# Kernel optimization log

Hardware: AMD Instinct MI355X
Metric: run time of the kernel (lower is better)

Reference implementation:

```python
import jax, jax.numpy as jnp
import numpy as np

T, B, I, H, P = 256, 128, 1024, 1024, 512  # seq, batch, input, hidden, proj


def setup_inputs() -> dict:
    key = jax.random.key(0)
    ks = jax.random.split(key, 6)
    s = 1.0 / np.sqrt(H)  # torch LSTM init bound: uniform(-1/sqrt(H), 1/sqrt(H))
    x = jax.random.normal(ks[0], (T, B, I), dtype=jnp.float32)
    h = jax.random.normal(ks[1], (1, B, P), dtype=jnp.float32) * 0.1
    c = jax.random.normal(ks[2], (1, B, H), dtype=jnp.float32) * 0.1
    W_ih = jax.random.uniform(ks[3], (4 * H, I), minval=-s, maxval=s, dtype=jnp.float32)
    W_hh = jax.random.uniform(ks[4], (4 * H, P), minval=-s, maxval=s, dtype=jnp.float32)
    W_hr = jax.random.uniform(ks[5], (P, H), minval=-s, maxval=s, dtype=jnp.float32)
    return {"x": x, "h": h, "c": c, "W_ih": W_ih, "W_hh": W_hh, "W_hr": W_hr}


def _lstm_proj(x, h0, c0, W_ih, W_hh, W_hr):
    # Precompute input contribution to gates for all timesteps: [T,B,4H]
    xg = jnp.einsum('tbi,gi->tbg', x, W_ih)

    def step(carry, xg_t):
        h_t, c_t = carry  # h_t:[B,P], c_t:[B,H]
        gates = xg_t + h_t @ W_hh.T  # [B,4H]
        i, f, g, o = jnp.split(gates, 4, axis=-1)  # torch gate order: i,f,g,o
        i = jax.nn.sigmoid(i)
        f = jax.nn.sigmoid(f)
        g = jnp.tanh(g)
        o = jax.nn.sigmoid(o)
        c_new = f * c_t + i * g
        h_full = o * jnp.tanh(c_new)        # [B,H]
        h_new = h_full @ W_hr.T             # projection -> [B,P]
        return (h_new, c_new), h_new

    (hT, cT), ys = jax.lax.scan(step, (h0[0], c0[0]), xg)
    return ys, hT[None, :, :], cT[None, :, :]


def reference(x, h, c, W_ih, W_hh, W_hr):
    return _lstm_proj(x, h, c, W_ih, W_hh, W_hr)
```

## Files before the change

kernel.cpp:

```cpp
#include <hip/hip_runtime.h>
#include <hip/hip_bf16.h>

#define TS 256
#define BB 128
#define II 1024
#define HH 1024
#define PP 512
#define GG 4096
#define NWG 256
#define WPG 64
#define BT 32
#define HCW 16
#define BSTRIDE 1032
#define RSTRIDE 20
#define SMEM_BYTES (64 * BSTRIDE * 2 + 2 * 64 * RSTRIDE * 4)

typedef __attribute__((ext_vector_type(8))) short bf16x8;
typedef __attribute__((ext_vector_type(4))) float f32x4;

__device__ __forceinline__ short f2bs(float f) {
    __hip_bfloat16 h = __float2bfloat16(f);
    return __builtin_bit_cast(short, h);
}
__device__ __forceinline__ float bs2f(short s) {
    return __bfloat162float(__builtin_bit_cast(__hip_bfloat16, s));
}

__device__ __forceinline__ bf16x8 ld8(const __hip_bfloat16* p) {
    return *(const bf16x8*)p;
}
__device__ __forceinline__ bf16x8 ld8(const float* p) {
    f32x4 lo = *(const f32x4*)p;
    f32x4 hi = *(const f32x4*)(p + 4);
    bf16x8 r;
#pragma unroll
    for (int i = 0; i < 4; ++i) { r[i] = f2bs(lo[i]); r[4 + i] = f2bs(hi[i]); }
    return r;
}

__device__ __forceinline__ void stv(float* p, long i, float v) { p[i] = v; }
__device__ __forceinline__ void stv(__hip_bfloat16* p, long i, float v) { p[i] = __float2bfloat16(v); }

__device__ __forceinline__ void st_bf16_wt(__hip_bfloat16* p, float v) {
    int si = (int)f2bs(v);
    asm volatile("global_store_short %0, %1, off sc1" :: "v"(p), "v"(si));
}
__device__ __forceinline__ f32x4 ld16_mall(const void* p) {
    f32x4 r;
    asm volatile("global_load_dwordx4 %0, %1, off sc1" : "=&v"(r) : "v"(p));
    return r;
}
__device__ __forceinline__ void vm_drain() {
    asm volatile("s_waitcnt vmcnt(0)" ::: "memory");
}

template <typename AT, typename BT_, typename CT>
__global__ __launch_bounds__(256) void mfma_gemm_bt(const AT* __restrict__ A,
                                                    const BT_* __restrict__ B,
                                                    CT* __restrict__ C,
                                                    int M, int N, int K) {
    __shared__ __align__(16) short As[128][40];
    __shared__ __align__(16) short Bsh[128][40];
    const int tid = threadIdx.x;
    const long bm = (long)blockIdx.y * 128;
    const long bn = (long)blockIdx.x * 128;
    const int lane = tid & 63, wv = tid >> 6;
    const int l15 = lane & 15, quad = lane >> 4;
    const int wm = (wv >> 1) * 64, wn = (wv & 1) * 64;
    f32x4 acc[4][4] = {};
    for (int k0 = 0; k0 < K; k0 += 32) {
#pragma unroll
        for (int i = 0; i < 2; ++i) {
            int ch = tid + 256 * i;
            int row = ch >> 2, koff = (ch & 3) * 8;
            *(bf16x8*)&As[row][koff] = ld8(&A[(bm + row) * (long)K + k0 + koff]);
            *(bf16x8*)&Bsh[row][koff] = ld8(&B[(bn + row) * (long)K + k0 + koff]);
        }
        __syncthreads();
        bf16x8 af[4], bfv[4];
#pragma unroll
        for (int t = 0; t < 4; ++t) {
            af[t] = *(const bf16x8*)&As[wm + t * 16 + l15][quad * 8];
            bfv[t] = *(const bf16x8*)&Bsh[wn + t * 16 + l15][quad * 8];
        }
#pragma unroll
        for (int mt = 0; mt < 4; ++mt)
#pragma unroll
            for (int nt = 0; nt < 4; ++nt)
                acc[mt][nt] = __builtin_amdgcn_mfma_f32_16x16x32_bf16(af[mt], bfv[nt], acc[mt][nt], 0, 0, 0);
        __syncthreads();
    }
#pragma unroll
    for (int mt = 0; mt < 4; ++mt)
#pragma unroll
        for (int nt = 0; nt < 4; ++nt)
#pragma unroll
            for (int r = 0; r < 4; ++r) {
                long row = bm + wm + mt * 16 + quad * 4 + r;
                long col = bn + wn + nt * 16 + l15;
                stv(C, row * N + col, acc[mt][nt][r]);
            }
}

template <int K>
__device__ __forceinline__ void rec_mm(const __hip_bfloat16* __restrict__ Abase,
                                       const short* __restrict__ Bs, f32x4* acc,
                                       int l15, int quad, int mt, int kh) {
    constexpr int KH = K / 2;
    constexpr int NI = KH / 32;
    const __hip_bfloat16* ap = Abase + (long)(mt * 16 + l15) * K + kh * KH + quad * 8;
    const short* bp0 = Bs + l15 * BSTRIDE + kh * KH + quad * 8;
    f32x4 avr[NI];
#pragma unroll
    for (int i = 0; i < NI; ++i) avr[i] = ld16_mall(ap + i * 32);
    asm volatile("s_waitcnt vmcnt(0)" ::: "memory");
    __builtin_amdgcn_sched_barrier(0);
#pragma unroll
    for (int i = 0; i < NI; ++i) {
        bf16x8 av = __builtin_bit_cast(bf16x8, avr[i]);
        const short* bp = bp0 + i * 32;
        acc[0] = __builtin_amdgcn_mfma_f32_16x16x32_bf16(av, *(const bf16x8*)(bp), acc[0], 0, 0, 0);
        acc[1] = __builtin_amdgcn_mfma_f32_16x16x32_bf16(av, *(const bf16x8*)(bp + 16 * BSTRIDE), acc[1], 0, 0, 0);
        acc[2] = __builtin_amdgcn_mfma_f32_16x16x32_bf16(av, *(const bf16x8*)(bp + 32 * BSTRIDE), acc[2], 0, 0, 0);
        acc[3] = __builtin_amdgcn_mfma_f32_16x16x32_bf16(av, *(const bf16x8*)(bp + 48 * BSTRIDE), acc[3], 0, 0, 0);
    }
}

__global__ __launch_bounds__(256) void lstm_rec_k(
    const __hip_bfloat16* __restrict__ h0b,
    const float* __restrict__ c0,
    const float* __restrict__ Whh,
    const __hip_bfloat16* __restrict__ Wcomb,
    const __hip_bfloat16* __restrict__ xg,
    __hip_bfloat16* __restrict__ hfull,
    float* __restrict__ cT,
    unsigned* __restrict__ flags) {
    extern __shared__ char smem[];
    short* Bs = (short*)smem;
    float* red = (float*)(smem + 64 * BSTRIDE * 2);

    const int tid = threadIdx.x;
    const int wg = blockIdx.x;
    const int grp = wg >> 6;
    const int jj = wg & 63;
    const int hc0 = jj * HCW;
    const int bt = grp * BT;
    const int lane = tid & 63, wv = tid >> 6;
    const int l15 = lane & 15, quad = lane >> 4;
    const int mt = wv & 1, kh = wv >> 1;
    unsigned* gflag = flags + grp * (2 * WPG);
    const int brow = bt + mt * 16 + quad * 4;

    for (int ch = tid; ch < 64 * 64; ch += 256) {
        int row = ch >> 6, koff = (ch & 63) * 8;
        long wr = (long)(row >> 4) * HH + hc0 + (row & 15);
        *(bf16x8*)&Bs[row * BSTRIDE + koff] = ld8(&Whh[wr * PP + koff]);
    }

    float creg[4];
    if (kh == 0) {
#pragma unroll
        for (int r = 0; r < 4; ++r) creg[r] = c0[(long)(brow + r) * HH + hc0 + l15];
    }

    short xr[16];
    auto ldxg = [&](int t) {
        if (kh == 0) {
            const __hip_bfloat16* xgt = xg + (long)t * BB * GG;
#pragma unroll
            for (int g = 0; g < 4; ++g)
#pragma unroll
                for (int r = 0; r < 4; ++r)
                    xr[g * 4 + r] = *(const short*)(xgt + (long)(brow + r) * GG + g * HH + hc0 + l15);
        }
    };

    auto wave_wait = [&](int want) {
        const unsigned* fp = gflag + mt * WPG + kh * 32;
        for (;;) {
            unsigned v = __hip_atomic_load(&fp[lane & 31], __ATOMIC_RELAXED,
                                           __HIP_MEMORY_SCOPE_AGENT);
            if (__all((int)(v >= (unsigned)want))) break;
            __builtin_amdgcn_s_sleep(1);
        }
    };

    auto finish = [&](f32x4* acc, int t, bool flag) {
        if (kh == 1) {
            float* rp = red + (mt * 64 + lane) * RSTRIDE;
#pragma unroll
            for (int g = 0; g < 4; ++g) *(f32x4*)(rp + g * 4) = acc[g];
        }
        __syncthreads();
        if (kh == 0) {
            const float* rp = red + (mt * 64 + lane) * RSTRIDE;
#pragma unroll
            for (int g = 0; g < 4; ++g) acc[g] += *(const f32x4*)(rp + g * 4);
            __hip_bfloat16* hp = hfull + (long)t * BB * HH;
#pragma unroll
            for (int r = 0; r < 4; ++r) {
                float gi = acc[0][r] + bs2f(xr[r]);
                float gf = acc[1][r] + bs2f(xr[4 + r]);
                float gg = acc[2][r] + bs2f(xr[8 + r]);
                float go = acc[3][r] + bs2f(xr[12 + r]);
                float i_ = 1.f / (1.f + expf(-gi));
                float f_ = 1.f / (1.f + expf(-gf));
                float g_ = tanhf(gg);
                float o_ = 1.f / (1.f + expf(-go));
                float c = f_ * creg[r] + i_ * g_;
                creg[r] = c;
                st_bf16_wt(hp + (long)(brow + r) * HH + hc0 + l15, o_ * tanhf(c));
            }
            vm_drain();
            if (flag && lane == 0) {
                __hip_atomic_store(&gflag[mt * WPG + jj], (unsigned)(t + 1),
                                   __ATOMIC_RELAXED, __HIP_MEMORY_SCOPE_AGENT);
            }
        }
    };

    ldxg(0);
    __syncthreads();
    {
        f32x4 acc[4] = {};
        rec_mm<PP>(h0b + (long)bt * PP, Bs, acc, l15, quad, mt, kh);
        finish(acc, 0, true);
    }
    for (int ch = tid; ch < 64 * 128; ch += 256) {
        int row = ch >> 7, koff = (ch & 127) * 8;
        long wr = (long)(row >> 4) * HH + hc0 + (row & 15);
        *(bf16x8*)&Bs[row * BSTRIDE + koff] = *(const bf16x8*)&Wcomb[wr * HH + koff];
    }
    __syncthreads();

    for (int t = 1; t < TS; ++t) {
        ldxg(t);
        wave_wait(t);
        f32x4 acc[4] = {};
        rec_mm<HH>(hfull + ((long)(t - 1) * BB + bt) * HH, Bs, acc, l15, quad, mt, kh);
        finish(acc, t, t < TS - 1);
    }

    if (kh == 0) {
#pragma unroll
        for (int r = 0; r < 4; ++r) cT[(long)(brow + r) * HH + hc0 + l15] = creg[r];
    }
}

__global__ __launch_bounds__(256) void prep_k(const float* __restrict__ h0,
                                              __hip_bfloat16* __restrict__ h0b,
                                              const float* __restrict__ Whr,
                                              float* __restrict__ WhrT,
                                              unsigned* __restrict__ flags) {
    int i = blockIdx.x * 256 + threadIdx.x;
    if (i < 2 * NWG) flags[i] = 0u;
    if (i < BB * PP) h0b[i] = __float2bfloat16(h0[i]);
    if (i < PP * HH) {
        int h = i / PP, p = i % PP;
        WhrT[i] = Whr[(long)p * HH + h];
    }
}

__global__ __launch_bounds__(256) void tail_k(const float* __restrict__ ys_last,
                                              float* __restrict__ hT) {
    int i = blockIdx.x * 256 + threadIdx.x;
    hT[i] = ys_last[i];
}

extern "C" void kernel_launch(void* const* d_in, const int* in_sizes, int n_in,
                              void* d_out, int out_size, void* d_ws, size_t ws_size,
                              hipStream_t stream) {
    const float* x   = (const float*)d_in[0];
    const float* h0  = (const float*)d_in[1];
    const float* c0  = (const float*)d_in[2];
    const float* Wih = (const float*)d_in[3];
    const float* Whh = (const float*)d_in[4];
    const float* Whr = (const float*)d_in[5];

    float* out = (float*)d_out;
    float* ys = out;
    float* hT = out + (long)TS * BB * PP;
    float* cT = hT + (long)BB * PP;

    char* ws = (char*)d_ws;
    size_t off = 0;
    __hip_bfloat16* xg = (__hip_bfloat16*)(ws + off);    off += (size_t)TS * BB * GG * 2;
    __hip_bfloat16* hfull = (__hip_bfloat16*)(ws + off); off += (size_t)TS * BB * HH * 2;
    __hip_bfloat16* Wcomb = (__hip_bfloat16*)(ws + off); off += (size_t)GG * HH * 2;
    float* WhrT = (float*)(ws + off);                    off += (size_t)HH * PP * 4;
    __hip_bfloat16* h0b = (__hip_bfloat16*)(ws + off);   off += (size_t)BB * PP * 2;
    unsigned* flags = (unsigned*)(ws + off);             off += 4096;

    static int smem_inited = 0;
    if (!smem_inited) {
        (void)hipFuncSetAttribute(reinterpret_cast<const void*>(lstm_rec_k),
                                  hipFuncAttributeMaxDynamicSharedMemorySize, SMEM_BYTES);
        smem_inited = 1;
    }

    dim3 blk(256);

    prep_k<<<dim3((PP * HH) / 256), blk, 0, stream>>>(h0, h0b, Whr, WhrT, flags);

    mfma_gemm_bt<float, float, __hip_bfloat16>
        <<<dim3(GG / 128, (TS * BB) / 128), blk, 0, stream>>>(x, Wih, xg, TS * BB, GG, II);

    mfma_gemm_bt<float, float, __hip_bfloat16>
        <<<dim3(HH / 128, GG / 128), blk, 0, stream>>>(Whh, WhrT, Wcomb, GG, HH, PP);

    {
        const __hip_bfloat16* a0 = h0b;
        const float* a1 = c0;
        const float* a2 = Whh;
        const __hip_bfloat16* a3 = Wcomb;
        const __hip_bfloat16* a4 = xg;
        __hip_bfloat16* a5 = hfull;
        float* a6 = cT;
        unsigned* a7 = flags;
        void* args[] = {(void*)&a0, (void*)&a1, (void*)&a2, (void*)&a3,
                        (void*)&a4, (void*)&a5, (void*)&a6, (void*)&a7};
        (void)hipLaunchCooperativeKernel(reinterpret_cast<void*>(lstm_rec_k),
                                         dim3(NWG), blk, args, SMEM_BYTES, stream);
    }

    mfma_gemm_bt<__hip_bfloat16, float, float>
        <<<dim3(PP / 128, (TS * BB) / 128), blk, 0, stream>>>(hfull, Whr, ys, TS * BB, PP, HH);

    tail_k<<<dim3((BB * PP) / 256), blk, 0, stream>>>(ys + (long)(TS - 1) * BB * PP, hT);
}
```

Before: 2.813 ms.

## Halve recurrent workgroups and drop split-K reduction with per-wave full-K rows

The persistent recurrent kernel now runs 128 workgroups in two batch groups of 64 rows instead of 256 workgroups in four groups. Each wave owns 16 batch rows and the full K dimension, so the LDS split-K reduction and the per-step __syncthreads go away, and each wave waits only on its own flags. Cache-policy bits on the h stores and loads also change from sc1 to sc0 sc1. The trade-off is twice the MFMA and load work per wave and half as many CUs in use, in exchange for less synchronisation on the serial critical path.

```diff
diff --git a/kernel.cpp b/kernel.cpp
--- a/kernel.cpp
+++ b/kernel.cpp
@@ -7,13 +7,14 @@
 #define HH 1024
 #define PP 512
 #define GG 4096
-#define NWG 256
+#define NWG 128
+#define NGRP 2
 #define WPG 64
-#define BT 32
+#define BT 64
 #define HCW 16
 #define BSTRIDE 1032
-#define RSTRIDE 20
-#define SMEM_BYTES (64 * BSTRIDE * 2 + 2 * 64 * RSTRIDE * 4)
+#define NFLAGS (NGRP * 4 * WPG)
+#define SMEM_BYTES (64 * BSTRIDE * 2)
 
 typedef __attribute__((ext_vector_type(8))) short bf16x8;
 typedef __attribute__((ext_vector_type(4))) float f32x4;
@@ -43,11 +44,11 @@
 
 __device__ __forceinline__ void st_bf16_wt(__hip_bfloat16* p, float v) {
     int si = (int)f2bs(v);
-    asm volatile("global_store_short %0, %1, off sc1" :: "v"(p), "v"(si));
+    asm volatile("global_store_short %0, %1, off sc0 sc1" :: "v"(p), "v"(si));
 }
 __device__ __forceinline__ f32x4 ld16_mall(const void* p) {
     f32x4 r;
-    asm volatile("global_load_dwordx4 %0, %1, off sc1" : "=&v"(r) : "v"(p));
+    asm volatile("global_load_dwordx4 %0, %1, off sc0 sc1" : "=&v"(r) : "v"(p));
     return r;
 }
 __device__ __forceinline__ void vm_drain() {
@@ -102,28 +103,11 @@
             }
 }
 
-template <int K>
-__device__ __forceinline__ void rec_mm(const __hip_bfloat16* __restrict__ Abase,
-                                       const short* __restrict__ Bs, f32x4* acc,
-                                       int l15, int quad, int mt, int kh) {
-    constexpr int KH = K / 2;
-    constexpr int NI = KH / 32;
-    const __hip_bfloat16* ap = Abase + (long)(mt * 16 + l15) * K + kh * KH + quad * 8;
-    const short* bp0 = Bs + l15 * BSTRIDE + kh * KH + quad * 8;
-    f32x4 avr[NI];
-#pragma unroll
-    for (int i = 0; i < NI; ++i) avr[i] = ld16_mall(ap + i * 32);
-    asm volatile("s_waitcnt vmcnt(0)" ::: "memory");
-    __builtin_amdgcn_sched_barrier(0);
-#pragma unroll
-    for (int i = 0; i < NI; ++i) {
-        bf16x8 av = __builtin_bit_cast(bf16x8, avr[i]);
-        const short* bp = bp0 + i * 32;
-        acc[0] = __builtin_amdgcn_mfma_f32_16x16x32_bf16(av, *(const bf16x8*)(bp), acc[0], 0, 0, 0);
-        acc[1] = __builtin_amdgcn_mfma_f32_16x16x32_bf16(av, *(const bf16x8*)(bp + 16 * BSTRIDE), acc[1], 0, 0, 0);
-        acc[2] = __builtin_amdgcn_mfma_f32_16x16x32_bf16(av, *(const bf16x8*)(bp + 32 * BSTRIDE), acc[2], 0, 0, 0);
-        acc[3] = __builtin_amdgcn_mfma_f32_16x16x32_bf16(av, *(const bf16x8*)(bp + 48 * BSTRIDE), acc[3], 0, 0, 0);
-    }
+__device__ __forceinline__ void mfma4(bf16x8 av, const short* bp, f32x4* acc) {
+    acc[0] = __builtin_amdgcn_mfma_f32_16x16x32_bf16(av, *(const bf16x8*)(bp), acc[0], 0, 0, 0);
+    acc[1] = __builtin_amdgcn_mfma_f32_16x16x32_bf16(av, *(const bf16x8*)(bp + 16 * BSTRIDE), acc[1], 0, 0, 0);
+    acc[2] = __builtin_amdgcn_mfma_f32_16x16x32_bf16(av, *(const bf16x8*)(bp + 32 * BSTRIDE), acc[2], 0, 0, 0);
+    acc[3] = __builtin_amdgcn_mfma_f32_16x16x32_bf16(av, *(const bf16x8*)(bp + 48 * BSTRIDE), acc[3], 0, 0, 0);
 }
 
 __global__ __launch_bounds__(256) void lstm_rec_k(
@@ -137,7 +121,6 @@
     unsigned* __restrict__ flags) {
     extern __shared__ char smem[];
     short* Bs = (short*)smem;
-    float* red = (float*)(smem + 64 * BSTRIDE * 2);
 
     const int tid = threadIdx.x;
     const int wg = blockIdx.x;
@@ -147,9 +130,10 @@
     const int bt = grp * BT;
     const int lane = tid & 63, wv = tid >> 6;
     const int l15 = lane & 15, quad = lane >> 4;
-    const int mt = wv & 1, kh = wv >> 1;
-    unsigned* gflag = flags + grp * (2 * WPG);
-    const int brow = bt + mt * 16 + quad * 4;
+    unsigned* fbase = flags + grp * (4 * WPG) + wv * WPG;
+    const int brow = bt + wv * 16 + quad * 4;
+    const int arow = bt + wv * 16 + l15;
+    const short* bp0 = Bs + l15 * BSTRIDE + quad * 8;
 
     for (int ch = tid; ch < 64 * 64; ch += 256) {
         int row = ch >> 6, koff = (ch & 63) * 8;
@@ -158,27 +142,22 @@
     }
 
     float creg[4];
-    if (kh == 0) {
-#pragma unroll
-        for (int r = 0; r < 4; ++r) creg[r] = c0[(long)(brow + r) * HH + hc0 + l15];
-    }
+#pragma unroll
+    for (int r = 0; r < 4; ++r) creg[r] = c0[(long)(brow + r) * HH + hc0 + l15];
 
     short xr[16];
     auto ldxg = [&](int t) {
-        if (kh == 0) {
-            const __hip_bfloat16* xgt = xg + (long)t * BB * GG;
-#pragma unroll
-            for (int g = 0; g < 4; ++g)
-#pragma unroll
-                for (int r = 0; r < 4; ++r)
-                    xr[g * 4 + r] = *(const short*)(xgt + (long)(brow + r) * GG + g * HH + hc0 + l15);
-        }
+        const __hip_bfloat16* xgt = xg + (long)t * BB * GG;
+#pragma unroll
+        for (int g = 0; g < 4; ++g)
+#pragma unroll
+            for (int r = 0; r < 4; ++r)
+                xr[g * 4 + r] = *(const short*)(xgt + (long)(brow + r) * GG + g * HH + hc0 + l15);
     };
 
     auto wave_wait = [&](int want) {
-        const unsigned* fp = gflag + mt * WPG + kh * 32;
         for (;;) {
-            unsigned v = __hip_atomic_load(&fp[lane & 31], __ATOMIC_RELAXED,
+            unsigned v = __hip_atomic_load(&fbase[lane], __ATOMIC_RELAXED,
                                            __HIP_MEMORY_SCOPE_AGENT);
             if (__all((int)(v >= (unsigned)want))) break;
             __builtin_amdgcn_s_sleep(1);
@@ -186,46 +165,48 @@
     };
 
     auto finish = [&](f32x4* acc, int t, bool flag) {
-        if (kh == 1) {
-            float* rp = red + (mt * 64 + lane) * RSTRIDE;
-#pragma unroll
-            for (int g = 0; g < 4; ++g) *(f32x4*)(rp + g * 4) = acc[g];
-        }
-        __syncthreads();
-        if (kh == 0) {
-            const float* rp = red + (mt * 64 + lane) * RSTRIDE;
-#pragma unroll
-            for (int g = 0; g < 4; ++g) acc[g] += *(const f32x4*)(rp + g * 4);
-            __hip_bfloat16* hp = hfull + (long)t * BB * HH;
-#pragma unroll
-            for (int r = 0; r < 4; ++r) {
-                float gi = acc[0][r] + bs2f(xr[r]);
-                float gf = acc[1][r] + bs2f(xr[4 + r]);
-                float gg = acc[2][r] + bs2f(xr[8 + r]);
-                float go = acc[3][r] + bs2f(xr[12 + r]);
-                float i_ = 1.f / (1.f + expf(-gi));
-                float f_ = 1.f / (1.f + expf(-gf));
-                float g_ = tanhf(gg);
-                float o_ = 1.f / (1.f + expf(-go));
-                float c = f_ * creg[r] + i_ * g_;
-                creg[r] = c;
-                st_bf16_wt(hp + (long)(brow + r) * HH + hc0 + l15, o_ * tanhf(c));
-            }
-            vm_drain();
-            if (flag && lane == 0) {
-                __hip_atomic_store(&gflag[mt * WPG + jj], (unsigned)(t + 1),
-                                   __ATOMIC_RELAXED, __HIP_MEMORY_SCOPE_AGENT);
-            }
-        }
+        __hip_bfloat16* hp = hfull + (long)t * BB * HH + (long)brow * HH + hc0 + l15;
+#pragma unroll
+        for (int r = 0; r < 4; ++r) {
+            float gi = acc[0][r] + bs2f(xr[r]);
+            float gf = acc[1][r] + bs2f(xr[4 + r]);
+            float gg = acc[2][r] + bs2f(xr[8 + r]);
+            float go = acc[3][r] + bs2f(xr[12 + r]);
+            float i_ = 1.f / (1.f + expf(-gi));
+            float f_ = 1.f / (1.f + expf(-gf));
+            float g_ = tanhf(gg);
+            float o_ = 1.f / (1.f + expf(-go));
+            float c = f_ * creg[r] + i_ * g_;
+            creg[r] = c;
+            st_bf16_wt(hp + (long)r * HH, o_ * tanhf(c));
+        }
+        vm_drain();
+        if (flag && lane == 0) {
+            __hip_atomic_store(&fbase[jj], (unsigned)(t + 1),
+                               __ATOMIC_RELAXED, __HIP_MEMORY_SCOPE_AGENT);
+        }
+    };
+
+    auto a_phase = [&](const __hip_bfloat16* ap, int c0_, f32x4* acc) {
+        f32x4 avr[16];
+#pragma unroll
+        for (int i = 0; i < 16; ++i) avr[i] = ld16_mall(ap + (c0_ + i) * 32);
+        asm volatile("s_waitcnt vmcnt(0)" ::: "memory");
+        __builtin_amdgcn_sched_barrier(0);
+#pragma unroll
+        for (int i = 0; i < 16; ++i)
+            mfma4(__builtin_bit_cast(bf16x8, avr[i]), bp0 + (c0_ + i) * 32, acc);
+        __builtin_amdgcn_sched_barrier(0);
     };
 
     ldxg(0);
     __syncthreads();
     {
         f32x4 acc[4] = {};
-        rec_mm<PP>(h0b + (long)bt * PP, Bs, acc, l15, quad, mt, kh);
+        a_phase(h0b + (long)arow * PP + quad * 8, 0, acc);
         finish(acc, 0, true);
     }
+    __syncthreads();
     for (int ch = tid; ch < 64 * 128; ch += 256) {
         int row = ch >> 7, koff = (ch & 127) * 8;
         long wr = (long)(row >> 4) * HH + hc0 + (row & 15);
@@ -236,15 +217,15 @@
     for (int t = 1; t < TS; ++t) {
         ldxg(t);
         wave_wait(t);
+        const __hip_bfloat16* ap = hfull + ((long)(t - 1) * BB + arow) * HH + quad * 8;
         f32x4 acc[4] = {};
-        rec_mm<HH>(hfull + ((long)(t - 1) * BB + bt) * HH, Bs, acc, l15, quad, mt, kh);
+        a_phase(ap, 0, acc);
+        a_phase(ap, 16, acc);
         finish(acc, t, t < TS - 1);
     }
 
-    if (kh == 0) {
-#pragma unroll
-        for (int r = 0; r < 4; ++r) cT[(long)(brow + r) * HH + hc0 + l15] = creg[r];
-    }
+#pragma unroll
+    for (int r = 0; r < 4; ++r) cT[(long)(brow + r) * HH + hc0 + l15] = creg[r];
 }
 
 __global__ __launch_bounds__(256) void prep_k(const float* __restrict__ h0,
@@ -253,7 +234,7 @@
                                               float* __restrict__ WhrT,
                                               unsigned* __restrict__ flags) {
     int i = blockIdx.x * 256 + threadIdx.x;
-    if (i < 2 * NWG) flags[i] = 0u;
+    if (i < NFLAGS) flags[i] = 0u;
     if (i < BB * PP) h0b[i] = __float2bfloat16(h0[i]);
     if (i < PP * HH) {
         int h = i / PP, p = i % PP;
```

New measurement: 3.421 ms. 21.6% more time.

## Remap recurrent workgroups across XCDs, pad h buffer, and use coherent loads

Applied to the files above, without the earlier changes.

Workgroup IDs are remapped so that each batch group's workgroups are interleaved across the chip's dies (bid&7 picks the group). The per-timestep hidden-state buffer is padded with an extra stride so consecutive timesteps do not alias. The cache-policy bits on the cross-workgroup h stores and loads are changed: stores now use sc0 sc1 and loads become plain global loads, with an acquire fence added at kernel start. The GEMM takes an explicit A tile stride so it can read the padded layout. It also adds some dead creg code. This risks coherence problems because the plain loads may hit stale L2 lines across dies.

```diff
diff --git a/kernel.cpp b/kernel.cpp
--- a/kernel.cpp
+++ b/kernel.cpp
@@ -8,11 +8,14 @@
 #define PP 512
 #define GG 4096
 #define NWG 256
+#define NGRP 4
 #define WPG 64
 #define BT 32
 #define HCW 16
 #define BSTRIDE 1032
 #define RSTRIDE 20
+#define HSTRIDE (BB * HH + 1024)
+#define NFLAGS (NGRP * 2 * WPG)
 #define SMEM_BYTES (64 * BSTRIDE * 2 + 2 * 64 * RSTRIDE * 4)
 
 typedef __attribute__((ext_vector_type(8))) short bf16x8;
@@ -43,11 +46,11 @@
 
 __device__ __forceinline__ void st_bf16_wt(__hip_bfloat16* p, float v) {
     int si = (int)f2bs(v);
-    asm volatile("global_store_short %0, %1, off sc1" :: "v"(p), "v"(si));
-}
-__device__ __forceinline__ f32x4 ld16_mall(const void* p) {
+    asm volatile("global_store_short %0, %1, off sc0 sc1" :: "v"(p), "v"(si));
+}
+__device__ __forceinline__ f32x4 ld16c(const void* p) {
     f32x4 r;
-    asm volatile("global_load_dwordx4 %0, %1, off sc1" : "=&v"(r) : "v"(p));
+    asm volatile("global_load_dwordx4 %0, %1, off" : "=&v"(r) : "v"(p));
     return r;
 }
 __device__ __forceinline__ void vm_drain() {
@@ -58,10 +61,12 @@
 __global__ __launch_bounds__(256) void mfma_gemm_bt(const AT* __restrict__ A,
                                                     const BT_* __restrict__ B,
                                                     CT* __restrict__ C,
-                                                    int M, int N, int K) {
+                                                    int M, int N, int K,
+                                                    long AtileStride) {
     __shared__ __align__(16) short As[128][40];
     __shared__ __align__(16) short Bsh[128][40];
     const int tid = threadIdx.x;
+    const long abase = (long)blockIdx.y * AtileStride;
     const long bm = (long)blockIdx.y * 128;
     const long bn = (long)blockIdx.x * 128;
     const int lane = tid & 63, wv = tid >> 6;
@@ -73,7 +78,7 @@
         for (int i = 0; i < 2; ++i) {
             int ch = tid + 256 * i;
             int row = ch >> 2, koff = (ch & 3) * 8;
-            *(bf16x8*)&As[row][koff] = ld8(&A[(bm + row) * (long)K + k0 + koff]);
+            *(bf16x8*)&As[row][koff] = ld8(&A[abase + row * (long)K + k0 + koff]);
             *(bf16x8*)&Bsh[row][koff] = ld8(&B[(bn + row) * (long)K + k0 + koff]);
         }
         __syncthreads();
@@ -112,7 +117,7 @@
     const short* bp0 = Bs + l15 * BSTRIDE + kh * KH + quad * 8;
     f32x4 avr[NI];
 #pragma unroll
-    for (int i = 0; i < NI; ++i) avr[i] = ld16_mall(ap + i * 32);
+    for (int i = 0; i < NI; ++i) avr[i] = ld16c(ap + i * 32);
     asm volatile("s_waitcnt vmcnt(0)" ::: "memory");
     __builtin_amdgcn_sched_barrier(0);
 #pragma unroll
@@ -139,10 +144,13 @@
     short* Bs = (short*)smem;
     float* red = (float*)(smem + 64 * BSTRIDE * 2);
 
+    __builtin_amdgcn_fence(__ATOMIC_ACQUIRE, "agent");
+
     const int tid = threadIdx.x;
-    const int wg = blockIdx.x;
-    const int grp = wg >> 6;
-    const int jj = wg & 63;
+    const int bid = blockIdx.x;
+    const int x8 = bid & 7;
+    const int grp = x8 >> 1;
+    const int jj = ((bid >> 3) << 1) | (x8 & 1);
     const int hc0 = jj * HCW;
     const int bt = grp * BT;
     const int lane = tid & 63, wv = tid >> 6;
@@ -157,10 +165,15 @@
         *(bf16x8*)&Bs[row * BSTRIDE + koff] = ld8(&Whh[wr * PP + koff]);
     }
 
-    float creg[4];
+    float creg[2];
+#pragma unroll
+    for (int i = 0; i < 2; ++i) creg[i] = 0.f;
     if (kh == 0) {
-#pragma unroll
-        for (int r = 0; r < 4; ++r) creg[r] = c0[(long)(brow + r) * HH + hc0 + l15];
+    }
+    float cregs[4];
+    if (kh == 0) {
+#pragma unroll
+        for (int r = 0; r < 4; ++r) cregs[r] = c0[(long)(brow + r) * HH + hc0 + l15];
     }
 
     short xr[16];
@@ -196,7 +209,7 @@
             const float* rp = red + (mt * 64 + lane) * RSTRIDE;
 #pragma unroll
             for (int g = 0; g < 4; ++g) acc[g] += *(const f32x4*)(rp + g * 4);
-            __hip_bfloat16* hp = hfull + (long)t * BB * HH;
+            __hip_bfloat16* hp = hfull + (long)t * HSTRIDE;
 #pragma unroll
             for (int r = 0; r < 4; ++r) {
                 float gi = acc[0][r] + bs2f(xr[r]);
@@ -207,8 +220,8 @@
                 float f_ = 1.f / (1.f + expf(-gf));
                 float g_ = tanhf(gg);
                 float o_ = 1.f / (1.f + expf(-go));
-                float c = f_ * creg[r] + i_ * g_;
-                creg[r] = c;
+                float c = f_ * cregs[r] + i_ * g_;
+                cregs[r] = c;
                 st_bf16_wt(hp + (long)(brow + r) * HH + hc0 + l15, o_ * tanhf(c));
             }
             vm_drain();
@@ -237,13 +250,13 @@
         ldxg(t);
         wave_wait(t);
         f32x4 acc[4] = {};
-        rec_mm<HH>(hfull + ((long)(t - 1) * BB + bt) * HH, Bs, acc, l15, quad, mt, kh);
+        rec_mm<HH>(hfull + (long)(t - 1) * HSTRIDE + (long)bt * HH, Bs, acc, l15, quad, mt, kh);
         finish(acc, t, t < TS - 1);
     }
 
     if (kh == 0) {
 #pragma unroll
-        for (int r = 0; r < 4; ++r) cT[(long)(brow + r) * HH + hc0 + l15] = creg[r];
+        for (int r = 0; r < 4; ++r) cT[(long)(brow + r) * HH + hc0 + l15] = cregs[r];
     }
 }
 
@@ -253,7 +266,7 @@
                                               float* __restrict__ WhrT,
                                               unsigned* __restrict__ flags) {
     int i = blockIdx.x * 256 + threadIdx.x;
-    if (i < 2 * NWG) flags[i] = 0u;
+    if (i < NFLAGS) flags[i] = 0u;
     if (i < BB * PP) h0b[i] = __float2bfloat16(h0[i]);
     if (i < PP * HH) {
         int h = i / PP, p = i % PP;
@@ -285,7 +298,7 @@
     char* ws = (char*)d_ws;
     size_t off = 0;
     __hip_bfloat16* xg = (__hip_bfloat16*)(ws + off);    off += (size_t)TS * BB * GG * 2;
-    __hip_bfloat16* hfull = (__hip_bfloat16*)(ws + off); off += (size_t)TS * BB * HH * 2;
+    __hip_bfloat16* hfull = (__hip_bfloat16*)(ws + off); off += (size_t)TS * HSTRIDE * 2;
     __hip_bfloat16* Wcomb = (__hip_bfloat16*)(ws + off); off += (size_t)GG * HH * 2;
     float* WhrT = (float*)(ws + off);                    off += (size_t)HH * PP * 4;
     __hip_bfloat16* h0b = (__hip_bfloat16*)(ws + off);   off += (size_t)BB * PP * 2;
@@ -303,10 +316,10 @@
     prep_k<<<dim3((PP * HH) / 256), blk, 0, stream>>>(h0, h0b, Whr, WhrT, flags);
 
     mfma_gemm_bt<float, float, __hip_bfloat16>
-        <<<dim3(GG / 128, (TS * BB) / 128), blk, 0, stream>>>(x, Wih, xg, TS * BB, GG, II);
+        <<<dim3(GG / 128, (TS * BB) / 128), blk, 0, stream>>>(x, Wih, xg, TS * BB, GG, II, 128L * II);
 
     mfma_gemm_bt<float, float, __hip_bfloat16>
-        <<<dim3(HH / 128, GG / 128), blk, 0, stream>>>(Whh, WhrT, Wcomb, GG, HH, PP);
+        <<<dim3(HH / 128, GG / 128), blk, 0, stream>>>(Whh, WhrT, Wcomb, GG, HH, PP, 128L * PP);
 
     {
         const __hip_bfloat16* a0 = h0b;
@@ -324,7 +337,7 @@
     }
 
     mfma_gemm_bt<__hip_bfloat16, float, float>
-        <<<dim3(PP / 128, (TS * BB) / 128), blk, 0, stream>>>(hfull, Whr, ys, TS * BB, PP, HH);
+        <<<dim3(PP / 128, (TS * BB) / 128), blk, 0, stream>>>(hfull, Whr, ys, TS * BB, PP, HH, (long)HSTRIDE);
 
     tail_k<<<dim3((BB * PP) / 256), blk, 0, stream>>>(ys + (long)(TS - 1) * BB * PP, hT);
 }
```

New measurement: 3.357 ms. +19.3%, slower.
